# Performance work log

Measured on AMD Instinct MI355X. Metric: run time of the kernel, lower is better.

Reference implementation:

```python
import jax, jax.numpy as jnp
import numpy as np

N, T, D = 2, 4096, 1024
H, E, L = 8, 4, 32
DK, DV = 64, 64

def setup_inputs():
    key = jax.random.key(0)
    ks = jax.random.split(key, 8)
    def randw(k, *d):
        return jax.random.normal(k, d, dtype=jnp.float32) / np.float32(np.sqrt(d[-1]))
    return {
        "X": jax.random.normal(ks[0], (N, T, D), dtype=jnp.float32),
        "w_G": randw(ks[1], H, E, D),
        "b_G": jnp.full((H, E), -float(H) ** 0.5, dtype=jnp.float32),
        "w_K": randw(ks[2], H, DK, D),
        "w_V": randw(ks[3], H, DV, D),
        "w_Q": randw(ks[4], H, DK, D),
        "w_O": randw(ks[5], DV * H, D),
        "init_K_rec": randw(ks[6], E, L, DK),
        "init_V_rec": randw(ks[7], E, L, DV),
    }

def _pscan(A, Xv, Y0):
    # Y_t = A_t * Y_{t-1} + X_t along axis 3 (chunk index), Y_{-1} = Y0
    Ae = jnp.broadcast_to(A[..., None], Xv.shape)
    Xv = Xv.at[..., 0, :].add(A[..., 0, None] * Y0)
    def op(c1, c2):
        a1, x1 = c1
        a2, x2 = c2
        return a1 * a2, a2 * x1 + x2
    _, Y = jax.lax.associative_scan(op, (Ae, Xv), axis=3)
    return Y

def reference(X, w_G, b_G, w_K, w_V, w_Q, w_O, init_K_rec, init_V_rec):
    n, t, _ = X.shape
    t_pad = ((t - 1) // L + 1) * L
    Xp = jnp.pad(X, ((0, 0), (0, t_pad - t), (0, 0)))
    # gates and projections
    G = jax.nn.sigmoid(jnp.einsum('ntd,hed->nhet', Xp, w_G) + b_G[None, :, :, None])
    K = jnp.einsum('ntc,hdc->nhtd', Xp, w_K)
    V = jnp.einsum('ntc,hdc->nhtd', Xp, w_V)
    A = 1.0 - jnp.minimum(G.sum(axis=1), 1.0)               # [n, E, t_pad]
    gK = jnp.einsum('nhet,nhtd->netd', G, K)
    gV = jnp.einsum('nhet,nhtd->netd', G, V)
    # split time as (L, t_pad//L): outer dim L, scan over chunk index (matches torch unflatten(2,(L,-1)))
    tc = t_pad // L
    A = A.reshape(n, E, L, tc)
    gK = gK.reshape(n, E, L, tc, DK)
    gV = gV.reshape(n, E, L, tc, DV)
    iK = jnp.broadcast_to(init_K_rec[None], (n, E, L, DK))
    iV = jnp.broadcast_to(init_V_rec[None], (n, E, L, DV))
    nK = _pscan(A, gK, iK).reshape(n, E, t_pad, DK)
    nV = _pscan(A, gV, iV).reshape(n, E, t_pad, DV)
    recK = jnp.concatenate([iK, nK], axis=2)                 # [n, E, L+t_pad, DK]
    recV = jnp.concatenate([iV, nV], axis=2)
    # moving window of size L ending at current position (slice starts at index 1 of rec buffer)
    idx = 1 + jnp.arange(t_pad)[:, None] + jnp.arange(L)[None, :]
    uk = recK[:, :, idx]                                     # [n, E, t_pad, L, DK]
    uv = recV[:, :, idx]                                     # [n, E, t_pad, L, DV]
    Q = jnp.einsum('ntc,hdc->nhtd', Xp, w_Q)
    scores = jnp.einsum('nhtd,netld->nhtel', Q, uk) / jnp.float32(np.sqrt(DK))
    probs = jax.nn.softmax(scores.reshape(n, H, t_pad, E * L), axis=-1).reshape(scores.shape)
    Y = jnp.einsum('nhtel,netld->nthd', probs, uv).reshape(n, t_pad, H * DV)
    return (Y @ w_O)[:, :t]
```

## Files before the change

kernel.cpp:

```cpp
#include <hip/hip_runtime.h>
#include <hip/hip_bf16.h>


using f4 = float4;
typedef __attribute__((ext_vector_type(8))) short short8;
typedef __attribute__((ext_vector_type(4))) float floatx4;

__device__ __forceinline__ ushort f2bf(float x) {
  unsigned u = __float_as_uint(x);
  u += 0x7fffu + ((u >> 16) & 1u);
  return (ushort)(u >> 16);
}
__device__ __forceinline__ unsigned pk2(float lo, float hi) {
  return (unsigned)f2bf(lo) | ((unsigned)f2bf(hi) << 16);
}

__device__ __forceinline__ void gll16(const void* g, void* l) {
  __builtin_amdgcn_global_load_lds((const __attribute__((address_space(1))) void*)g,
                                   (__attribute__((address_space(3))) void*)l, 16, 0, 0);
}

__global__ __launch_bounds__(256)
void conv_f32_bf16(const float* __restrict__ src, ushort* __restrict__ dst, int n4) {
  for (int i = blockIdx.x * blockDim.x + threadIdx.x; i < n4; i += gridDim.x * blockDim.x) {
    f4 v = ((const f4*)src)[i];
    ushort4 o; o.x = f2bf(v.x); o.y = f2bf(v.y); o.z = f2bf(v.z); o.w = f2bf(v.w);
    ((ushort4*)dst)[i] = o;
  }
}

__global__ __launch_bounds__(256)
void conv_weights(const float* __restrict__ wK, const float* __restrict__ wV,
                  const float* __restrict__ wQ, const float* __restrict__ wG,
                  ushort* __restrict__ wAll) {
  int i4 = blockIdx.x * 256 + threadIdx.x;
  int idx = i4 * 4;
  int row = idx >> 10;
  f4 v = make_float4(0.f, 0.f, 0.f, 0.f);
  if (row < 512)       v = *(const f4*)&wK[idx];
  else if (row < 1024) v = *(const f4*)&wV[idx - 524288];
  else if (row < 1536) v = *(const f4*)&wQ[idx - 1048576];
  else if (row < 1568) v = *(const f4*)&wG[idx - 1572864];
  ushort4 o; o.x = f2bf(v.x); o.y = f2bf(v.y); o.z = f2bf(v.z); o.w = f2bf(v.w);
  *(ushort4*)&wAll[idx] = o;
}

__global__ __launch_bounds__(256)
void transpose_wO(const float* __restrict__ wO, ushort* __restrict__ wObf) {
  int i = blockIdx.x * 256 + threadIdx.x;
  int n = i >> 9, k = i & 511;
  wObf[i] = f2bf(wO[(size_t)k * 1024 + n]);
}

#define GSTEP(LDA_, WAITS, STAGE_, KT) do {                                       \
  asm volatile("s_waitcnt vmcnt(" WAITS ")" ::: "memory");                        \
  __builtin_amdgcn_s_barrier();                                                   \
  if (STAGE_) {                                                                   \
    const ushort* ga = gA + (size_t)((KT) + 2) * 32;                              \
    const ushort* gb = gB + (size_t)((KT) + 2) * 32;                              \
    ushort* la = As + ss * 4096 + tid * 8;                                        \
    ushort* lb = Bs + ss * 4096 + tid * 8;                                        \
    gll16(ga, la); gll16(ga + 64 * (LDA_), la + 2048);                            \
    gll16(gb, lb); gll16(gb + 64 * (LDA_), lb + 2048);                            \
  }                                                                               \
  {                                                                               \
    const ushort* Afp = As + cs * 4096 + (wm + l15) * 32 + koff;                  \
    const ushort* Bfp = Bs + cs * 4096 + (wn + l15) * 32 + koff;                  \
    short8 bf_[4];                                                                \
    _Pragma("unroll")                                                             \
    for (int ni = 0; ni < 4; ni++) bf_[ni] = *(const short8*)(Bfp + ni * 512);    \
    __builtin_amdgcn_s_setprio(1);                                                \
    _Pragma("unroll")                                                             \
    for (int mi = 0; mi < 4; mi++) {                                              \
      short8 af_ = *(const short8*)(Afp + mi * 512);                              \
      _Pragma("unroll")                                                           \
      for (int ni = 0; ni < 4; ni++)                                              \
        acc[mi][ni] = __builtin_amdgcn_mfma_f32_16x16x32_bf16(                    \
            af_, bf_[ni], acc[mi][ni], 0, 0, 0);                                  \
    }                                                                             \
    __builtin_amdgcn_s_setprio(0);                                                \
    cs = (cs == 2) ? 0 : cs + 1;                                                  \
    ss = (ss == 2) ? 0 : ss + 1;                                                  \
  }                                                                               \
} while (0)

__global__ __launch_bounds__(256, 3)
void proj_gemm_128s(const ushort* __restrict__ Xbf, const ushort* __restrict__ wAll,
                    float* __restrict__ Kp, float* __restrict__ Vp,
                    ushort* __restrict__ Qbf, float* __restrict__ Glin)
{
  __shared__ ushort As[3 * 4096];
  __shared__ ushort Bs[3 * 4096];

  const int tid = threadIdx.x;
  const int bid = blockIdx.x;
  const int xcd = bid & 7, slot = bid >> 3;
  const int ct = slot % 13;
  const int my = xcd * 8 + slot / 13;
  const int m0 = my * 128, n0 = ct * 128;

  const int lane = tid & 63, w = tid >> 6;
  const int wm = (w >> 1) * 64, wn = (w & 1) * 64;
  const int l15 = lane & 15, lg = lane >> 4;
  const int fl = (l15 & 3) ^ ((l15 >> 2) & 3);
  const int koff = ((lg ^ fl) & 3) * 8;

  const int srow = tid >> 2;
  const int schunk = (tid & 3) ^ ((srow & 3) ^ ((srow >> 2) & 3));
  const ushort* gA = Xbf  + (size_t)(m0 + srow) * 1024 + schunk * 8;
  const ushort* gB = wAll + (size_t)(n0 + srow) * 1024 + schunk * 8;

  floatx4 acc[4][4];
#pragma unroll
  for (int mi = 0; mi < 4; mi++)
#pragma unroll
    for (int ni = 0; ni < 4; ni++) acc[mi][ni] = (floatx4){0.f, 0.f, 0.f, 0.f};

#pragma unroll
  for (int t_ = 0; t_ < 2; t_++) {
    const ushort* ga = gA + t_ * 32;
    const ushort* gb = gB + t_ * 32;
    ushort* la = As + t_ * 4096 + tid * 8;
    ushort* lb = Bs + t_ * 4096 + tid * 8;
    gll16(ga, la); gll16(ga + 65536, la + 2048);
    gll16(gb, lb); gll16(gb + 65536, lb + 2048);
  }
  int cs = 0, ss = 2;

#pragma unroll 1
  for (int kt = 0; kt < 31; ++kt) GSTEP(1024, "4", kt <= 29, kt);
  GSTEP(1024, "0", false, 31);

#pragma unroll
  for (int mi = 0; mi < 4; mi++) {
    const int rm = m0 + wm + mi * 16 + lg * 4;
#pragma unroll
    for (int ni = 0; ni < 4; ni++) {
      const int Cg = n0 + wn + ni * 16 + l15;
#pragma unroll
      for (int j = 0; j < 4; j++) {
        const float v = acc[mi][ni][j];
        if (Cg < 512)        Kp [(size_t)(rm + j) * 512 + Cg] = v;
        else if (Cg < 1024)  Vp [(size_t)(rm + j) * 512 + Cg - 512] = v;
        else if (Cg < 1536)  Qbf[(size_t)(rm + j) * 512 + Cg - 1024] = f2bf(v * 0.125f);
        else if (Cg < 1568)  Glin[(size_t)(rm + j) * 32 + Cg - 1536] = v;
      }
    }
  }
}

__global__ __launch_bounds__(256, 3)
void out_gemm_128s(const ushort* __restrict__ Ybf, const ushort* __restrict__ wObf,
                   float* __restrict__ out)
{
  __shared__ ushort As[3 * 4096];
  __shared__ ushort Bs[3 * 4096];

  const int tid = threadIdx.x;
  const int bid = blockIdx.x;
  const int xcd = bid & 7, slot = bid >> 3;
  const int ct = slot & 7;
  const int my = xcd * 8 + (slot >> 3);
  const int m0 = my * 128, n0 = ct * 128;

  const int lane = tid & 63, w = tid >> 6;
  const int wm = (w >> 1) * 64, wn = (w & 1) * 64;
  const int l15 = lane & 15, lg = lane >> 4;
  const int fl = (l15 & 3) ^ ((l15 >> 2) & 3);
  const int koff = ((lg ^ fl) & 3) * 8;

  const int srow = tid >> 2;
  const int schunk = (tid & 3) ^ ((srow & 3) ^ ((srow >> 2) & 3));
  const ushort* gA = Ybf  + (size_t)(m0 + srow) * 512 + schunk * 8;
  const ushort* gB = wObf + (size_t)(n0 + srow) * 512 + schunk * 8;

  floatx4 acc[4][4];
#pragma unroll
  for (int mi = 0; mi < 4; mi++)
#pragma unroll
    for (int ni = 0; ni < 4; ni++) acc[mi][ni] = (floatx4){0.f, 0.f, 0.f, 0.f};

#pragma unroll
  for (int t_ = 0; t_ < 2; t_++) {
    const ushort* ga = gA + t_ * 32;
    const ushort* gb = gB + t_ * 32;
    ushort* la = As + t_ * 4096 + tid * 8;
    ushort* lb = Bs + t_ * 4096 + tid * 8;
    gll16(ga, la); gll16(ga + 32768, la + 2048);
    gll16(gb, lb); gll16(gb + 32768, lb + 2048);
  }
  int cs = 0, ss = 2;

#pragma unroll 1
  for (int kt = 0; kt < 15; ++kt) GSTEP(512, "4", kt <= 13, kt);
  GSTEP(512, "0", false, 15);

#pragma unroll
  for (int mi = 0; mi < 4; mi++) {
    const int rm = m0 + wm + mi * 16 + lg * 4;
#pragma unroll
    for (int ni = 0; ni < 4; ni++) {
      const int cn = n0 + wn + ni * 16 + l15;
#pragma unroll
      for (int j = 0; j < 4; j++)
        out[(size_t)(rm + j) * 1024 + cn] = acc[mi][ni][j];
    }
  }
}

__global__ __launch_bounds__(256)
void gate_kernel(const float* __restrict__ Glin, const float* __restrict__ bG,
                 const float* __restrict__ Kp, const float* __restrict__ Vp,
                 float* __restrict__ gK, float* __restrict__ gV, float* __restrict__ Aout)
{
  const int nt = blockIdx.x * 4 + (threadIdx.x >> 6);
  const int lane = threadIdx.x & 63;
  const int n = nt >> 12;
  const int t = nt & 4095;

  float g[32];
  float gsum[4] = {0.f, 0.f, 0.f, 0.f};
#pragma unroll
  for (int f = 0; f < 32; f++) {
    float z = Glin[(size_t)nt * 32 + f] + bG[f];
    float s = 1.f / (1.f + __expf(-z));
    g[f] = s;
    gsum[f & 3] += s;
  }
  if (lane < 4) {
    float a = 1.f - fminf(gsum[lane], 1.f);
    Aout[(size_t)(n * 4 + lane) * 4096 + t] = a;
  }
  float gk[4] = {0.f, 0.f, 0.f, 0.f}, gv[4] = {0.f, 0.f, 0.f, 0.f};
#pragma unroll
  for (int h = 0; h < 8; h++) {
    float kv = Kp[(size_t)nt * 512 + h * 64 + lane];
    float vv = Vp[(size_t)nt * 512 + h * 64 + lane];
#pragma unroll
    for (int e = 0; e < 4; e++) {
      gk[e] = fmaf(g[h * 4 + e], kv, gk[e]);
      gv[e] = fmaf(g[h * 4 + e], vv, gv[e]);
    }
  }
#pragma unroll
  for (int e = 0; e < 4; e++) {
    size_t base = ((size_t)(n * 4 + e) * 4096 + t) * 64 + lane;
    gK[base] = gk[e];
    gV[base] = gv[e];
  }
}

__global__ __launch_bounds__(64)
void scan_kernel(float* __restrict__ gK, float* __restrict__ gV,
                 const float* __restrict__ Aarr,
                 const float* __restrict__ initK, const float* __restrict__ initV)
{
  __shared__ float sB[128 * 64];
  __shared__ float sA[128];
  const int b = blockIdx.x;
  const int half = b >> 8, sub = b & 255;
  float* gX = half ? gV : gK;
  const float* initX = half ? initV : initK;
  const int n = sub >> 7, r = sub & 127, e = r >> 5, l = r & 31;
  const int tbase = l * 128;
  const size_t base = ((size_t)(n * 4 + e) * 4096 + tbase) * 64;
  const int tid = threadIdx.x;

  const f4* src = (const f4*)&gX[base];
#pragma unroll
  for (int q = 0; q < 32; q++)
    *(f4*)&sB[(tid + q * 64) * 4] = src[tid + q * 64];
  sA[tid]      = Aarr[(size_t)(n * 4 + e) * 4096 + tbase + tid];
  sA[64 + tid] = Aarr[(size_t)(n * 4 + e) * 4096 + tbase + 64 + tid];
  __syncthreads();

  float state = initX[((size_t)e * 32 + l) * 64 + tid];
  float* dst = &gX[base];
  for (int c = 0; c < 128; c++) {
    state = fmaf(sA[c], state, sB[c * 64 + tid]);
    dst[c * 64 + tid] = state;
  }
}

__global__ __launch_bounds__(256, 1)
void attn_mfma(const ushort* __restrict__ Qbf, const float* __restrict__ nK,
               const float* __restrict__ nV, const float* __restrict__ initK,
               const float* __restrict__ initV, ushort* __restrict__ Yout)
{
  __shared__ ushort Kw[4][4096];
  __shared__ ushort Vt[4][4096];
  __shared__ ushort Pl[4][4096];

  const int blk = blockIdx.x;
  const int n = blk >> 7, c = blk & 127;
  const int t0 = c * 32;
  const int tid = threadIdx.x;
  const int lane = tid & 63;
  const int w = tid >> 6;
  const int l15 = lane & 15, lg = lane >> 4;

  short8 qf[4][2];
#pragma unroll
  for (int mi = 0; mi < 4; mi++) {
    int m = w * 64 + mi * 16 + l15;
    int t = t0 + (m & 31), h = m >> 5;
    const ushort* src = &Qbf[((size_t)(n * 4096 + t)) * 512 + h * 64];
#pragma unroll
    for (int kk = 0; kk < 2; kk++)
      qf[mi][kk] = *(const short8*)&src[kk * 32 + lg * 8];
  }

#pragma unroll 4
  for (int it = 0; it < 16; it++) {
    int idx = it * 256 + tid;
    int e = idx >> 10, u = (idx >> 4) & 63, d = (idx & 15) * 4;
    int s = t0 - 31 + u;
    int scl = s < 4095 ? s : 4095;
    const float* pK = (s >= 0) ? &nK[(((size_t)(n * 4 + e)) * 4096 + scl) * 64 + d]
                               : &initK[((size_t)e * 32 + (s + 32)) * 64 + d];
    const float* pV = (s >= 0) ? &nV[(((size_t)(n * 4 + e)) * 4096 + scl) * 64 + d]
                               : &initV[((size_t)e * 32 + (s + 32)) * 64 + d];
    f4 kv = *(const f4*)pK;
    f4 vv = *(const f4*)pV;
    if (u == 63) { kv = make_float4(0.f,0.f,0.f,0.f); vv = make_float4(0.f,0.f,0.f,0.f); }
    uint2 kp; kp.x = pk2(kv.x, kv.y); kp.y = pk2(kv.z, kv.w);
    int ka = (u * 128 + d * 2) ^ ((u & 7) << 4);
    *(uint2*)((char*)&Kw[e][0] + ka) = kp;
    ushort vb[4] = { f2bf(vv.x), f2bf(vv.y), f2bf(vv.z), f2bf(vv.w) };
#pragma unroll
    for (int q = 0; q < 4; q++) {
      int dq = d + q;
      int va = (dq * 128 + u * 2) ^ ((dq & 7) << 4);
      *(ushort*)((char*)&Vt[e][0] + va) = vb[q];
    }
  }
  __syncthreads();

  floatx4 Yacc[4][4];
#pragma unroll
  for (int mi = 0; mi < 4; mi++)
#pragma unroll
    for (int nd = 0; nd < 4; nd++) Yacc[mi][nd] = (floatx4){0.f,0.f,0.f,0.f};
  float mrun[4][4], lrun[4][4];
#pragma unroll
  for (int mi = 0; mi < 4; mi++)
#pragma unroll
    for (int r = 0; r < 4; r++) { mrun[mi][r] = -1e30f; lrun[mi][r] = 0.f; }

  const floatx4 zf = (floatx4){0.f,0.f,0.f,0.f};
  char* pb = (char*)&Pl[w][0];

#pragma unroll
  for (int half = 0; half < 2; half++) {
    floatx4 S[2][4][4];
#pragma unroll
    for (int ep = 0; ep < 2; ep++) {
      const int e = half * 2 + ep;
#pragma unroll
      for (int ni = 0; ni < 4; ni++) {
        const int urow = ni * 16 + l15;
        const int sw = (urow & 7) << 4;
        short8 kf0 = *(const short8*)((const char*)&Kw[e][0] + ((urow * 128 + lg * 16) ^ sw));
        short8 kf1 = *(const short8*)((const char*)&Kw[e][0] + ((urow * 128 + 64 + lg * 16) ^ sw));
#pragma unroll
        for (int mi = 0; mi < 4; mi++) {
          floatx4 t_ = __builtin_amdgcn_mfma_f32_16x16x32_bf16(qf[mi][0], kf0, zf, 0, 0, 0);
          S[ep][mi][ni] = __builtin_amdgcn_mfma_f32_16x16x32_bf16(qf[mi][1], kf1, t_, 0, 0, 0);
        }
      }
    }
#pragma unroll
    for (int mi = 0; mi < 4; mi++)
#pragma unroll
      for (int r = 0; r < 4; r++) {
        const int iq = (mi & 1) * 16 + lg * 4 + r;
        float mx = mrun[mi][r];
#pragma unroll
        for (int ep = 0; ep < 2; ep++)
#pragma unroll
          for (int ni = 0; ni < 4; ni++) {
            const int u = ni * 16 + l15;
            float v = ((unsigned)(u - iq) < 32u) ? S[ep][mi][ni][r] : -1e30f;
            S[ep][mi][ni][r] = v;
            mx = fmaxf(mx, v);
          }
        mx = fmaxf(mx, __shfl_xor(mx, 1));
        mx = fmaxf(mx, __shfl_xor(mx, 2));
        mx = fmaxf(mx, __shfl_xor(mx, 4));
        mx = fmaxf(mx, __shfl_xor(mx, 8));
        float sc = __expf(mrun[mi][r] - mx);
        mrun[mi][r] = mx;
        float sum = 0.f;
#pragma unroll
        for (int ep = 0; ep < 2; ep++)
#pragma unroll
          for (int ni = 0; ni < 4; ni++) {
            float p = __expf(S[ep][mi][ni][r] - mx);
            S[ep][mi][ni][r] = p;
            sum += p;
          }
        sum += __shfl_xor(sum, 1);
        sum += __shfl_xor(sum, 2);
        sum += __shfl_xor(sum, 4);
        sum += __shfl_xor(sum, 8);
        lrun[mi][r] = lrun[mi][r] * sc + sum;
#pragma unroll
        for (int nd = 0; nd < 4; nd++) Yacc[mi][nd][r] *= sc;
      }
#pragma unroll
    for (int ep = 0; ep < 2; ep++) {
      const int e = half * 2 + ep;
#pragma unroll
      for (int mi = 0; mi < 4; mi++)
#pragma unroll
        for (int r = 0; r < 4; r++) {
          const int m = mi * 16 + lg * 4 + r;
          const int base = m * 128, sw = (m & 7) << 4;
#pragma unroll
          for (int ni = 0; ni < 4; ni++) {
            const int u = ni * 16 + l15;
            *(ushort*)(pb + ((base + u * 2) ^ sw)) = f2bf(S[ep][mi][ni][r]);
          }
        }
      asm volatile("s_waitcnt lgkmcnt(0)" ::: "memory");
      __builtin_amdgcn_sched_barrier(0);
#pragma unroll
      for (int kk = 0; kk < 2; kk++) {
        short8 pa[4];
#pragma unroll
        for (int mi = 0; mi < 4; mi++) {
          const int m = mi * 16 + l15;
          pa[mi] = *(const short8*)(pb + ((m * 128 + kk * 64 + lg * 16) ^ ((m & 7) << 4)));
        }
#pragma unroll
        for (int nd = 0; nd < 4; nd++) {
          const int dr = nd * 16 + l15;
          short8 vf = *(const short8*)((const char*)&Vt[e][0] +
                        ((dr * 128 + kk * 64 + lg * 16) ^ ((dr & 7) << 4)));
#pragma unroll
          for (int mi = 0; mi < 4; mi++)
            Yacc[mi][nd] = __builtin_amdgcn_mfma_f32_16x16x32_bf16(pa[mi], vf, Yacc[mi][nd], 0, 0, 0);
        }
      }
    }
  }

#pragma unroll
  for (int mi = 0; mi < 4; mi++)
#pragma unroll
    for (int r = 0; r < 4; r++) {
      const float inv = 1.f / lrun[mi][r];
      const int m = w * 64 + mi * 16 + lg * 4 + r;
      const int t = t0 + (m & 31), h = m >> 5;
      ushort* dst = &Yout[((size_t)(n * 4096 + t)) * 512 + h * 64];
#pragma unroll
      for (int nd = 0; nd < 4; nd++)
        dst[nd * 16 + l15] = f2bf(Yacc[mi][nd][r] * inv);
    }
}

extern "C" void kernel_launch(void* const* d_in, const int* in_sizes, int n_in,
                              void* d_out, int out_size, void* d_ws, size_t ws_size,
                              hipStream_t stream) {
  const float* X     = (const float*)d_in[0];
  const float* wG    = (const float*)d_in[1];
  const float* bG    = (const float*)d_in[2];
  const float* wK    = (const float*)d_in[3];
  const float* wV    = (const float*)d_in[4];
  const float* wQ    = (const float*)d_in[5];
  const float* wO    = (const float*)d_in[6];
  const float* initK = (const float*)d_in[7];
  const float* initV = (const float*)d_in[8];
  float* out = (float*)d_out;

  float* ws = (float*)d_ws;
  ushort* Xbf  = (ushort*)(ws + 0);
  float*  gK   = ws + 0;
  float*  gV   = ws + 2097152;
  ushort* wAll = (ushort*)(ws + 4194304);
  ushort* wObf = (ushort*)(ws + 5111808);
  float*  Glin = ws + 5373952;
  float*  Kp   = ws + 5636096;
  ushort* Ybf  = (ushort*)Kp;
  float*  Vp   = ws + 9830400;
  ushort* Qbf  = (ushort*)(ws + 14024704);
  float*  Aarr = ws + 16121856;

  conv_f32_bf16<<<2048, 256, 0, stream>>>(X, Xbf, 2097152);
  conv_weights<<<1664, 256, 0, stream>>>(wK, wV, wQ, wG, wAll);
  transpose_wO<<<2048, 256, 0, stream>>>(wO, wObf);
  proj_gemm_128s<<<832, 256, 0, stream>>>(Xbf, wAll, Kp, Vp, Qbf, Glin);
  gate_kernel<<<2048, 256, 0, stream>>>(Glin, bG, Kp, Vp, gK, gV, Aarr);
  scan_kernel<<<512, 64, 0, stream>>>(gK, gV, Aarr, initK, initV);
  attn_mfma<<<256, 256, 0, stream>>>(Qbf, gK, gV, initK, initV, Ybf);
  out_gemm_128s<<<512, 256, 0, stream>>>(Ybf, wObf, out);
}
```

Measured before the change: 221.1 us.

## Split attention over experts across 8 waves and merge three prep kernels

The attention kernel now runs 512 threads per block. Each group of four waves handles half of the experts, and the two partial softmax states are combined through LDS at the end with a log-sum-exp merge. This doubles the wave-level parallelism per block, since only 256 blocks are launched on a many-CU GPU. The three conversion kernels for X, the weights and the transposed w_O are fused into one launch to cut launch overhead. The cost is more LDS (8 P buffers plus the exchange) and an extra merge phase with two barriers.

Result: slower. 237.4 us (+7.4%).

```diff
diff --git a/kernel.cpp b/kernel.cpp
--- a/kernel.cpp
+++ b/kernel.cpp
@@ -21,35 +21,39 @@
 }
 
 __global__ __launch_bounds__(256)
-void conv_f32_bf16(const float* __restrict__ src, ushort* __restrict__ dst, int n4) {
-  for (int i = blockIdx.x * blockDim.x + threadIdx.x; i < n4; i += gridDim.x * blockDim.x) {
-    f4 v = ((const f4*)src)[i];
+void prep_kernel(const float* __restrict__ X,
+                 const float* __restrict__ wK, const float* __restrict__ wV,
+                 const float* __restrict__ wQ, const float* __restrict__ wG,
+                 const float* __restrict__ wO,
+                 ushort* __restrict__ Xbf, ushort* __restrict__ wAll,
+                 ushort* __restrict__ wObf)
+{
+  const int b = blockIdx.x;
+  if (b < 2048) {
+    int i0 = b * 256 + threadIdx.x;
+#pragma unroll
+    for (int k = 0; k < 4; k++) {
+      int idx = i0 + k * 524288;
+      f4 v = ((const f4*)X)[idx];
+      ushort4 o; o.x = f2bf(v.x); o.y = f2bf(v.y); o.z = f2bf(v.z); o.w = f2bf(v.w);
+      ((ushort4*)Xbf)[idx] = o;
+    }
+  } else if (b < 3712) {
+    int i4 = (b - 2048) * 256 + threadIdx.x;
+    int idx = i4 * 4;
+    int row = idx >> 10;
+    f4 v = make_float4(0.f, 0.f, 0.f, 0.f);
+    if (row < 512)       v = *(const f4*)&wK[idx];
+    else if (row < 1024) v = *(const f4*)&wV[idx - 524288];
+    else if (row < 1536) v = *(const f4*)&wQ[idx - 1048576];
+    else if (row < 1568) v = *(const f4*)&wG[idx - 1572864];
     ushort4 o; o.x = f2bf(v.x); o.y = f2bf(v.y); o.z = f2bf(v.z); o.w = f2bf(v.w);
-    ((ushort4*)dst)[i] = o;
-  }
-}
-
-__global__ __launch_bounds__(256)
-void conv_weights(const float* __restrict__ wK, const float* __restrict__ wV,
-                  const float* __restrict__ wQ, const float* __restrict__ wG,
-                  ushort* __restrict__ wAll) {
-  int i4 = blockIdx.x * 256 + threadIdx.x;
-  int idx = i4 * 4;
-  int row = idx >> 10;
-  f4 v = make_float4(0.f, 0.f, 0.f, 0.f);
-  if (row < 512)       v = *(const f4*)&wK[idx];
-  else if (row < 1024) v = *(const f4*)&wV[idx - 524288];
-  else if (row < 1536) v = *(const f4*)&wQ[idx - 1048576];
-  else if (row < 1568) v = *(const f4*)&wG[idx - 1572864];
-  ushort4 o; o.x = f2bf(v.x); o.y = f2bf(v.y); o.z = f2bf(v.z); o.w = f2bf(v.w);
-  *(ushort4*)&wAll[idx] = o;
-}
-
-__global__ __launch_bounds__(256)
-void transpose_wO(const float* __restrict__ wO, ushort* __restrict__ wObf) {
-  int i = blockIdx.x * 256 + threadIdx.x;
-  int n = i >> 9, k = i & 511;
-  wObf[i] = f2bf(wO[(size_t)k * 1024 + n]);
+    *(ushort4*)&wAll[idx] = o;
+  } else {
+    int i = (b - 3712) * 256 + threadIdx.x;
+    int n = i >> 9, k = i & 511;
+    wObf[i] = f2bf(wO[(size_t)k * 1024 + n]);
+  }
 }
 
 #define GSTEP(LDA_, WAITS, STAGE_, KT) do {                                       \
@@ -282,14 +286,16 @@
   }
 }
 
-__global__ __launch_bounds__(256, 1)
-void attn_mfma(const ushort* __restrict__ Qbf, const float* __restrict__ nK,
-               const float* __restrict__ nV, const float* __restrict__ initK,
-               const float* __restrict__ initV, ushort* __restrict__ Yout)
+__global__ __launch_bounds__(512, 1)
+void attn_mfma8(const ushort* __restrict__ Qbf, const float* __restrict__ nK,
+                const float* __restrict__ nV, const float* __restrict__ initK,
+                const float* __restrict__ initV, ushort* __restrict__ Yout)
 {
   __shared__ ushort Kw[4][4096];
   __shared__ ushort Vt[4][4096];
-  __shared__ ushort Pl[4][4096];
+  __shared__ ushort Pl[8][4096];
+  __shared__ float sM[4][64];
+  __shared__ float sL[4][64];
 
   const int blk = blockIdx.x;
   const int n = blk >> 7, c = blk & 127;
@@ -297,12 +303,14 @@
   const int tid = threadIdx.x;
   const int lane = tid & 63;
   const int w = tid >> 6;
+  const int w4 = w & 3;
+  const int hv = w >> 2;
   const int l15 = lane & 15, lg = lane >> 4;
 
   short8 qf[4][2];
 #pragma unroll
   for (int mi = 0; mi < 4; mi++) {
-    int m = w * 64 + mi * 16 + l15;
+    int m = w4 * 64 + mi * 16 + l15;
     int t = t0 + (m & 31), h = m >> 5;
     const ushort* src = &Qbf[((size_t)(n * 4096 + t)) * 512 + h * 64];
 #pragma unroll
@@ -311,8 +319,8 @@
   }
 
 #pragma unroll 4
-  for (int it = 0; it < 16; it++) {
-    int idx = it * 256 + tid;
+  for (int it = 0; it < 8; it++) {
+    int idx = it * 512 + tid;
     int e = idx >> 10, u = (idx >> 4) & 63, d = (idx & 15) * 4;
     int s = t0 - 31 + u;
     int scl = s < 4095 ? s : 4095;
@@ -350,12 +358,11 @@
   const floatx4 zf = (floatx4){0.f,0.f,0.f,0.f};
   char* pb = (char*)&Pl[w][0];
 
-#pragma unroll
-  for (int half = 0; half < 2; half++) {
+  {
     floatx4 S[2][4][4];
 #pragma unroll
     for (int ep = 0; ep < 2; ep++) {
-      const int e = half * 2 + ep;
+      const int e = hv * 2 + ep;
 #pragma unroll
       for (int ni = 0; ni < 4; ni++) {
         const int urow = ni * 16 + l15;
@@ -388,7 +395,6 @@
         mx = fmaxf(mx, __shfl_xor(mx, 2));
         mx = fmaxf(mx, __shfl_xor(mx, 4));
         mx = fmaxf(mx, __shfl_xor(mx, 8));
-        float sc = __expf(mrun[mi][r] - mx);
         mrun[mi][r] = mx;
         float sum = 0.f;
 #pragma unroll
@@ -403,13 +409,11 @@
         sum += __shfl_xor(sum, 2);
         sum += __shfl_xor(sum, 4);
         sum += __shfl_xor(sum, 8);
-        lrun[mi][r] = lrun[mi][r] * sc + sum;
-#pragma unroll
-        for (int nd = 0; nd < 4; nd++) Yacc[mi][nd][r] *= sc;
+        lrun[mi][r] = sum;
       }
 #pragma unroll
     for (int ep = 0; ep < 2; ep++) {
-      const int e = half * 2 + ep;
+      const int e = hv * 2 + ep;
 #pragma unroll
       for (int mi = 0; mi < 4; mi++)
 #pragma unroll
@@ -445,18 +449,42 @@
     }
   }
 
-#pragma unroll
-  for (int mi = 0; mi < 4; mi++)
-#pragma unroll
-    for (int r = 0; r < 4; r++) {
-      const float inv = 1.f / lrun[mi][r];
-      const int m = w * 64 + mi * 16 + lg * 4 + r;
-      const int t = t0 + (m & 31), h = m >> 5;
-      ushort* dst = &Yout[((size_t)(n * 4096 + t)) * 512 + h * 64];
-#pragma unroll
-      for (int nd = 0; nd < 4; nd++)
-        dst[nd * 16 + l15] = f2bf(Yacc[mi][nd][r] * inv);
-    }
+  __syncthreads();
+  float* exch = (float*)&Pl[0][0];
+  if (w >= 4) {
+#pragma unroll
+    for (int mi = 0; mi < 4; mi++)
+#pragma unroll
+      for (int r = 0; r < 4; r++) {
+        const int m4 = mi * 16 + lg * 4 + r;
+        if (l15 == 0) { sM[w4][m4] = mrun[mi][r]; sL[w4][m4] = lrun[mi][r]; }
+#pragma unroll
+        for (int nd = 0; nd < 4; nd++)
+          exch[w4 * 4096 + m4 * 64 + nd * 16 + l15] = Yacc[mi][nd][r];
+      }
+  }
+  __syncthreads();
+  if (w < 4) {
+#pragma unroll
+    for (int mi = 0; mi < 4; mi++)
+#pragma unroll
+      for (int r = 0; r < 4; r++) {
+        const int m4 = mi * 16 + lg * 4 + r;
+        const float m1 = sM[w4][m4], l1 = sL[w4][m4];
+        const float m0 = mrun[mi][r], l0 = lrun[mi][r];
+        const float mm = fmaxf(m0, m1);
+        const float a0 = __expf(m0 - mm), a1 = __expf(m1 - mm);
+        const float inv = 1.f / (l0 * a0 + l1 * a1);
+        const int m = w4 * 64 + m4;
+        const int t = t0 + (m & 31), h = m >> 5;
+        ushort* dst = &Yout[((size_t)(n * 4096 + t)) * 512 + h * 64];
+#pragma unroll
+        for (int nd = 0; nd < 4; nd++) {
+          const float y1 = exch[w4 * 4096 + m4 * 64 + nd * 16 + l15];
+          dst[nd * 16 + l15] = f2bf((Yacc[mi][nd][r] * a0 + y1 * a1) * inv);
+        }
+      }
+  }
 }
 
 extern "C" void kernel_launch(void* const* d_in, const int* in_sizes, int n_in,
@@ -486,12 +514,10 @@
   ushort* Qbf  = (ushort*)(ws + 14024704);
   float*  Aarr = ws + 16121856;
 
-  conv_f32_bf16<<<2048, 256, 0, stream>>>(X, Xbf, 2097152);
-  conv_weights<<<1664, 256, 0, stream>>>(wK, wV, wQ, wG, wAll);
-  transpose_wO<<<2048, 256, 0, stream>>>(wO, wObf);
+  prep_kernel<<<5760, 256, 0, stream>>>(X, wK, wV, wQ, wG, wO, Xbf, wAll, wObf);
   proj_gemm_128s<<<832, 256, 0, stream>>>(Xbf, wAll, Kp, Vp, Qbf, Glin);
   gate_kernel<<<2048, 256, 0, stream>>>(Glin, bG, Kp, Vp, gK, gV, Aarr);
   scan_kernel<<<512, 64, 0, stream>>>(gK, gV, Aarr, initK, initV);
-  attn_mfma<<<256, 256, 0, stream>>>(Qbf, gK, gV, initK, initV, Ybf);
+  attn_mfma8<<<256, 512, 0, stream>>>(Qbf, gK, gV, initK, initV, Ybf);
   out_gemm_128s<<<512, 256, 0, stream>>>(Ybf, wObf, out);
 }
```
